# Optimization experiments

Measured on AMD Instinct MI355X. Metric: run time of the kernel, lower is better.

Reference implementation:

```python
import jax, jax.numpy as jnp
import numpy as np

KL_W, SIZ_W, DEN_W, MAT_W = 0.001, 0.05, 0.1, 0.1


def setup_inputs() -> dict:
    key = jax.random.key(0)
    ks = jax.random.split(key, 9)
    B, N, M, L = 4, 8192, 8192, 512
    return {
        "pred_pos": jax.random.normal(ks[0], (B, N, 3), jnp.float32),
        "pred_sizing": jax.random.normal(ks[1], (B, N, 1), jnp.float32),
        "pred_material": jax.random.normal(ks[2], (B, N, 4), jnp.float32),
        "target_pos": jax.random.normal(ks[3], (B, M, 3), jnp.float32),
        "target_sizing": jax.random.normal(ks[4], (B, N, 1), jnp.float32),
        "target_material": jax.random.normal(ks[5], (B, N, 4), jnp.float32),
        "mu": jax.random.normal(ks[6], (B, L), jnp.float32),
        "logvar": jax.random.normal(ks[7], (B, L), jnp.float32),
        "sub_idx": jax.random.randint(ks[8], (1024,), 0, N, jnp.int64),
    }


def _pairwise_sq(a, b):
    # squared euclidean distances: [B,N,M]
    a2 = jnp.sum(a * a, axis=-1)                     # [B,N]
    b2 = jnp.sum(b * b, axis=-1)                     # [B,M]
    ab = jnp.einsum('bnd,bmd->bnm', a, b)            # [B,N,M]
    return a2[:, :, None] + b2[:, None, :] - 2.0 * ab


def reference(pred_pos, pred_sizing, pred_material, target_pos,
              target_sizing, target_material, mu, logvar, sub_idx):
    # Chamfer: one pairwise matrix, min over both axes
    d = _pairwise_sq(pred_pos, target_pos)           # [B,N,M]
    cd = (jnp.min(d, axis=2).mean(axis=1) + jnp.min(d, axis=1).mean(axis=1)).mean()

    # KL divergence term
    kl = -0.5 * jnp.mean(1.0 + logvar - mu ** 2 - jnp.exp(logvar))

    # density uniformity on a 1024-point subsample
    pts = pred_pos[:, sub_idx]                       # [B,n,3]
    n = pts.shape[1]
    dd = _pairwise_sq(pts, pts) + jnp.eye(n, dtype=pts.dtype)[None] * 1e6
    nn_d = jnp.min(dd, axis=2)                       # [B,n]
    density = jnp.std(nn_d, axis=1, ddof=1).mean()   # torch .std is unbiased

    sizing_loss = jnp.mean((pred_sizing - target_sizing) ** 2)
    material_loss = jnp.mean((pred_material - target_material) ** 2)

    total = cd + KL_W * kl + DEN_W * density + SIZ_W * sizing_loss + MAT_W * material_loss
    return total
```

## Files before the change

### kernel.cpp

```cpp
#include <hip/hip_runtime.h>
#include <math.h>

#define BB 4
#define NN 8192
#define LL 512
#define NSUB 1024

#define AUX_BLOCKS 64
#define SL_BLOCKS 48
#define CH_BLOCKS 1024
#define PREP_BLOCKS 256

#define PPS_OFF 0
#define CHS_OFF 256
#define DNS_OFF 1280
#define KL_OFF  1312
#define SIZ_OFF 1360
#define MAT_OFF 1408
#define FRAG_OFF ((size_t)8192)
#define FRAG_SET ((size_t)BB * NN * 32)

typedef __bf16 bf16x8 __attribute__((ext_vector_type(8)));
typedef float f32x16 __attribute__((ext_vector_type(16)));

__device__ inline unsigned short f2bf(float f) {
    unsigned u = __float_as_uint(f);
    unsigned r = (u + 0x7FFFu + ((u >> 16) & 1u)) >> 16;
    return (unsigned short)r;
}
__device__ inline float bf2f(unsigned short h) {
    return __uint_as_float(((unsigned)h) << 16);
}
__device__ inline unsigned pk(unsigned short lo, unsigned short hi) {
    return (unsigned)lo | ((unsigned)hi << 16);
}

__device__ inline float blockReduceSum256(float v) {
    __shared__ float red[4];
    #pragma unroll
    for (int o = 32; o; o >>= 1) v += __shfl_down(v, o);
    __syncthreads();
    if ((threadIdx.x & 63) == 0) red[threadIdx.x >> 6] = v;
    __syncthreads();
    return red[0] + red[1] + red[2] + red[3];
}

__global__ __launch_bounds__(256) void prep_frags_kernel(
    const float* __restrict__ pred, const float* __restrict__ targ,
    unsigned char* __restrict__ frag, float* __restrict__ ws) {
    const int i = blockIdx.x * 256 + threadIdx.x;
    const int s = i >> 15;
    const int r = i & (BB * NN - 1);
    const int b = r >> 13;
    const int p = r & (NN - 1);
    const float* pos = (s ? targ : pred) + (size_t)r * 3;
    const float x = pos[0], y = pos[1], z = pos[2];
    const unsigned short hx = f2bf(x), hy = f2bf(y), hz = f2bf(z);
    const unsigned short lx = f2bf(x - bf2f(hx));
    const unsigned short ly = f2bf(y - bf2f(hy));
    const unsigned short lz = f2bf(z - bf2f(hz));
    const float pp = fmaf(x, x, fmaf(y, y, z * z));
    const float w = -0.5f * pp;
    const unsigned short wh = f2bf(w);
    const float wr = w - bf2f(wh);
    const unsigned short wl = f2bf(wr);
    const unsigned short wl2 = f2bf(wr - bf2f(wl));
    const unsigned short ONE = 0x3F80;

    uint4 a0, a1, b0, b1;
    a0.x = pk(hx, hy); a0.y = pk(hz, lx); a0.z = pk(ly, lz); a0.w = pk(hx, hy);
    a1.x = pk(hz, lx); a1.y = pk(ly, lz); a1.z = pk(ONE, ONE); a1.w = pk(ONE, 0);
    b0.x = pk(hx, hy); b0.y = pk(hz, hx); b0.z = pk(hy, hz); b0.w = pk(lx, ly);
    b1.x = pk(lz, lx); b1.y = pk(ly, lz); b1.z = pk(wh, wl); b1.w = pk(wl2, 0);

    uint4* Adst = (uint4*)(frag + (size_t)s * FRAG_SET) + (size_t)r * 2;
    Adst[0] = a0;
    Adst[1] = a1;
    uint4* Bdst = (uint4*)(frag + (2 + s) * FRAG_SET);
    const size_t bi = (size_t)b * NN * 2 + (size_t)(p >> 5) * 64 + (p & 31);
    Bdst[bi] = b0;
    Bdst[bi + 32] = b1;

    float sum = blockReduceSum256(pp);
    if (threadIdx.x == 0) ws[PPS_OFF + blockIdx.x] = sum;
}

__global__ __launch_bounds__(256, 4) void mega_kernel(
    const float* __restrict__ pred,
    const unsigned char* __restrict__ frag,
    const float* __restrict__ mu, const float* __restrict__ logvar,
    const float* __restrict__ psiz, const float* __restrict__ tsiz,
    const float* __restrict__ pmat, const float* __restrict__ tmat,
    const int* __restrict__ sub_idx, float* __restrict__ ws) {
    __shared__ __align__(16) unsigned char smem[16384];
    const int tid = threadIdx.x;
    const int bid = blockIdx.x;

    if (bid >= AUX_BLOCKS) {
        const int cid = bid - AUX_BLOCKS;
        const int bd = cid & 7;
        const int rg = cid >> 3;
        const int b = bd >> 1;
        const int dir = bd & 1;
        const int As = dir;
        const int Bs = dir ^ 1;
        const int w = tid >> 6, lane = tid & 63;
        const int lo5 = lane & 31, sel = lane >> 5;

        const uint4* Ap = (const uint4*)(frag + (size_t)As * FRAG_SET) +
                          (size_t)b * NN * 2;
        const int qbase = rg * 64;
        const bf16x8 A0 = __builtin_bit_cast(
            bf16x8, Ap[(size_t)(qbase + lo5) * 2 + sel]);
        const bf16x8 A1 = __builtin_bit_cast(
            bf16x8, Ap[(size_t)(qbase + 32 + lo5) * 2 + sel]);

        const uint4* Bq = (const uint4*)(frag + (size_t)(2 + Bs) * FRAG_SET) +
                          (size_t)b * NN * 2 + (size_t)w * 4096 + lane;

        f32x16 st0, st1;
        #pragma unroll
        for (int i = 0; i < 16; ++i) { st0[i] = -3e38f; st1[i] = -3e38f; }
        const f32x16 zc = {};

        uint4 c0 = Bq[0], c1 = Bq[64];
        uint4 n0 = Bq[128], n1 = Bq[192];
        #pragma unroll 1
        for (int it = 0; it < 32; ++it) {
            const int pf = (it < 30) ? (it + 2) : it;
            uint4 m0 = Bq[(size_t)pf * 128];
            uint4 m1 = Bq[(size_t)pf * 128 + 64];
            const bf16x8 B0 = __builtin_bit_cast(bf16x8, c0);
            const bf16x8 B1 = __builtin_bit_cast(bf16x8, c1);
            {
                f32x16 d0 = __builtin_amdgcn_mfma_f32_32x32x16_bf16(
                    A0, B0, zc, 0, 0, 0);
                f32x16 d1 = __builtin_amdgcn_mfma_f32_32x32x16_bf16(
                    A0, B1, zc, 0, 0, 0);
                #pragma unroll
                for (int i = 0; i < 16; ++i)
                    st0[i] = fmaxf(fmaxf(st0[i], d0[i]), d1[i]);
            }
            {
                f32x16 e0 = __builtin_amdgcn_mfma_f32_32x32x16_bf16(
                    A1, B0, zc, 0, 0, 0);
                f32x16 e1 = __builtin_amdgcn_mfma_f32_32x32x16_bf16(
                    A1, B1, zc, 0, 0, 0);
                #pragma unroll
                for (int i = 0; i < 16; ++i)
                    st1[i] = fmaxf(fmaxf(st1[i], e0[i]), e1[i]);
            }
            c0 = n0; c1 = n1;
            n0 = m0; n1 = m1;
        }

        #pragma unroll
        for (int m = 1; m <= 16; m <<= 1) {
            #pragma unroll
            for (int i = 0; i < 16; ++i) {
                st0[i] = fmaxf(st0[i], __shfl_xor(st0[i], m));
                st1[i] = fmaxf(st1[i], __shfl_xor(st1[i], m));
            }
        }
        float* sm = (float*)smem;
        if (lo5 == 0) {
            #pragma unroll
            for (int i = 0; i < 16; ++i) {
                const int r = (i & 3) + 8 * (i >> 2) + 4 * sel;
                sm[w * 64 + r] = st0[i];
                sm[w * 64 + 32 + r] = st1[i];
            }
        }
        __syncthreads();
        if (tid < 64) {
            float v = fmaxf(fmaxf(sm[tid], sm[64 + tid]),
                            fmaxf(sm[128 + tid], sm[192 + tid]));
            #pragma unroll
            for (int o = 32; o; o >>= 1) v += __shfl_down(v, o);
            if (tid == 0) ws[CHS_OFF + cid] = v;
        }
        return;
    }

    if (bid < 16) {
        float4* pts = (float4*)smem;
        const int chunk = bid & 3;
        const int b = bid >> 2;
        for (int k = tid; k < NSUB; k += 256) {
            int idx = sub_idx[k];
            const float* p = pred + ((size_t)b * NN + idx) * 3;
            float x = p[0], y = p[1], z = p[2];
            pts[k] = make_float4(x, y, z, -0.5f * fmaf(x, x, fmaf(y, y, z * z)));
        }
        __syncthreads();
        const int i = chunk * 256 + tid;
        const float4 me = pts[i];
        float h0 = -1e30f, h1 = -1e30f, h2 = -1e30f, h3 = -1e30f;
        #pragma unroll 4
        for (int j = 0; j < NSUB; j += 4) {
            float4 q0 = pts[j + 0], q1 = pts[j + 1], q2 = pts[j + 2], q3 = pts[j + 3];
            float t0 = fmaf(me.z, q0.z, q0.w);
            t0 = fmaf(me.y, q0.y, t0); t0 = fmaf(me.x, q0.x, t0);
            t0 = (j + 0 == i) ? -1e30f : t0; h0 = fmaxf(h0, t0);
            float t1 = fmaf(me.z, q1.z, q1.w);
            t1 = fmaf(me.y, q1.y, t1); t1 = fmaf(me.x, q1.x, t1);
            t1 = (j + 1 == i) ? -1e30f : t1; h1 = fmaxf(h1, t1);
            float t2 = fmaf(me.z, q2.z, q2.w);
            t2 = fmaf(me.y, q2.y, t2); t2 = fmaf(me.x, q2.x, t2);
            t2 = (j + 2 == i) ? -1e30f : t2; h2 = fmaxf(h2, t2);
            float t3 = fmaf(me.z, q3.z, q3.w);
            t3 = fmaf(me.y, q3.y, t3); t3 = fmaf(me.x, q3.x, t3);
            t3 = (j + 3 == i) ? -1e30f : t3; h3 = fmaxf(h3, t3);
        }
        float h = fmaxf(fmaxf(h0, h1), fmaxf(h2, h3));
        float pp = fmaf(me.x, me.x, fmaf(me.y, me.y, me.z * me.z));
        float m = pp - 2.0f * h;
        float s = blockReduceSum256(m); __syncthreads();
        float ss = blockReduceSum256(m * m);
        if (tid == 0) {
            ws[DNS_OFF + bid] = s;
            ws[DNS_OFF + 16 + bid] = ss;
        }
    } else {
        const int r = bid - 16;
        const int stride = SL_BLOCKS * 256;
        const int g0 = r * 256 + tid;
        float skl = 0.0f;
        for (int i = g0; i < BB * LL; i += stride) {
            float m = mu[i], lv = logvar[i];
            skl += 1.0f + lv - m * m - expf(lv);
        }
        float ssz = 0.0f;
        for (int i = g0; i < BB * NN; i += stride) {
            float d = psiz[i] - tsiz[i];
            ssz = fmaf(d, d, ssz);
        }
        float smt = 0.0f;
        for (int i = g0; i < BB * NN * 4; i += stride) {
            float d = pmat[i] - tmat[i];
            smt = fmaf(d, d, smt);
        }
        skl = blockReduceSum256(skl); __syncthreads();
        ssz = blockReduceSum256(ssz); __syncthreads();
        smt = blockReduceSum256(smt);
        if (tid == 0) {
            ws[KL_OFF + r] = skl;
            ws[SIZ_OFF + r] = ssz;
            ws[MAT_OFF + r] = smt;
        }
    }
}

__global__ __launch_bounds__(256) void finalize_kernel(
    const float* __restrict__ ws, float* __restrict__ out) {
    const int t = threadIdx.x;
    float pp = ws[PPS_OFF + t];
    float ch = ws[CHS_OFF + t] + ws[CHS_OFF + 256 + t] +
               ws[CHS_OFF + 512 + t] + ws[CHS_OFF + 768 + t];
    float kl = (t < SL_BLOCKS) ? ws[KL_OFF + t] : 0.0f;
    float sz = (t < SL_BLOCKS) ? ws[SIZ_OFF + t] : 0.0f;
    float mt = (t < SL_BLOCKS) ? ws[MAT_OFF + t] : 0.0f;
    float s_pp = blockReduceSum256(pp); __syncthreads();
    float s_ch = blockReduceSum256(ch); __syncthreads();
    float s_kl = blockReduceSum256(kl); __syncthreads();
    float s_sz = blockReduceSum256(sz); __syncthreads();
    float s_mt = blockReduceSum256(mt);
    if (t == 0) {
        float den = 0.0f;
        #pragma unroll
        for (int b = 0; b < BB; ++b) {
            float s = ws[DNS_OFF + 4 * b + 0] + ws[DNS_OFF + 4 * b + 1] +
                      ws[DNS_OFF + 4 * b + 2] + ws[DNS_OFF + 4 * b + 3];
            float q = ws[DNS_OFF + 16 + 4 * b + 0] + ws[DNS_OFF + 16 + 4 * b + 1] +
                      ws[DNS_OFF + 16 + 4 * b + 2] + ws[DNS_OFF + 16 + 4 * b + 3];
            float var = (q - s * s / (float)NSUB) / (float)(NSUB - 1);
            den += sqrtf(fmaxf(var, 0.0f));
        }
        den *= (1.0f / BB);
        float cd = (s_pp - 2.0f * s_ch) / (float)(BB * NN);
        float klv = -0.5f * s_kl / (float)(BB * LL);
        float sizing = s_sz / (float)(BB * NN);
        float material = s_mt / (float)(BB * NN * 4);
        out[0] = cd + 0.001f * klv + 0.1f * den + 0.05f * sizing +
                 0.1f * material;
    }
}

extern "C" void kernel_launch(void* const* d_in, const int* in_sizes, int n_in,
                              void* d_out, int out_size, void* d_ws,
                              size_t ws_size, hipStream_t stream) {
    const float* pred_pos = (const float*)d_in[0];
    const float* pred_siz = (const float*)d_in[1];
    const float* pred_mat = (const float*)d_in[2];
    const float* targ_pos = (const float*)d_in[3];
    const float* targ_siz = (const float*)d_in[4];
    const float* targ_mat = (const float*)d_in[5];
    const float* mu = (const float*)d_in[6];
    const float* logvar = (const float*)d_in[7];
    const int* sub_idx = (const int*)d_in[8];
    float* out = (float*)d_out;
    float* ws = (float*)d_ws;
    unsigned char* frag = (unsigned char*)d_ws + FRAG_OFF;

    prep_frags_kernel<<<PREP_BLOCKS, 256, 0, stream>>>(pred_pos, targ_pos,
                                                       frag, ws);
    mega_kernel<<<AUX_BLOCKS + CH_BLOCKS, 256, 0, stream>>>(
        pred_pos, frag, mu, logvar, pred_siz, targ_siz, pred_mat, targ_mat,
        sub_idx, ws);
    finalize_kernel<<<1, 256, 0, stream>>>(ws, out);
}
```

Measured before the change: 42.28 us.

## Move aux work into prep kernel and give chamfer its own kernel

The density and small-loss (KL, sizing, material) blocks move out of the chamfer mega-kernel into the prep kernel. Chamfer then runs as a dedicated kernel with a lean 1 KB shared buffer instead of 16 KB. Its block index mapping also changes so consecutive blocks share the same batch and direction, which should improve L2 reuse of the B fragments. This removes the imbalance of aux blocks competing with MFMA blocks, at the cost of a longer prep kernel.

```diff
diff --git a/kernel.cpp b/kernel.cpp
--- a/kernel.cpp
+++ b/kernel.cpp
@@ -6,10 +6,10 @@
 #define LL 512
 #define NSUB 1024
 
-#define AUX_BLOCKS 64
 #define SL_BLOCKS 48
 #define CH_BLOCKS 1024
-#define PREP_BLOCKS 256
+#define PREP_BLOCKS 320
+#define RED_BLOCKS 64
 
 #define PPS_OFF 0
 #define CHS_OFF 256
@@ -45,147 +45,57 @@
     return red[0] + red[1] + red[2] + red[3];
 }
 
-__global__ __launch_bounds__(256) void prep_frags_kernel(
+__global__ __launch_bounds__(256) void prep_kernel(
     const float* __restrict__ pred, const float* __restrict__ targ,
-    unsigned char* __restrict__ frag, float* __restrict__ ws) {
-    const int i = blockIdx.x * 256 + threadIdx.x;
-    const int s = i >> 15;
-    const int r = i & (BB * NN - 1);
-    const int b = r >> 13;
-    const int p = r & (NN - 1);
-    const float* pos = (s ? targ : pred) + (size_t)r * 3;
-    const float x = pos[0], y = pos[1], z = pos[2];
-    const unsigned short hx = f2bf(x), hy = f2bf(y), hz = f2bf(z);
-    const unsigned short lx = f2bf(x - bf2f(hx));
-    const unsigned short ly = f2bf(y - bf2f(hy));
-    const unsigned short lz = f2bf(z - bf2f(hz));
-    const float pp = fmaf(x, x, fmaf(y, y, z * z));
-    const float w = -0.5f * pp;
-    const unsigned short wh = f2bf(w);
-    const float wr = w - bf2f(wh);
-    const unsigned short wl = f2bf(wr);
-    const unsigned short wl2 = f2bf(wr - bf2f(wl));
-    const unsigned short ONE = 0x3F80;
-
-    uint4 a0, a1, b0, b1;
-    a0.x = pk(hx, hy); a0.y = pk(hz, lx); a0.z = pk(ly, lz); a0.w = pk(hx, hy);
-    a1.x = pk(hz, lx); a1.y = pk(ly, lz); a1.z = pk(ONE, ONE); a1.w = pk(ONE, 0);
-    b0.x = pk(hx, hy); b0.y = pk(hz, hx); b0.z = pk(hy, hz); b0.w = pk(lx, ly);
-    b1.x = pk(lz, lx); b1.y = pk(ly, lz); b1.z = pk(wh, wl); b1.w = pk(wl2, 0);
-
-    uint4* Adst = (uint4*)(frag + (size_t)s * FRAG_SET) + (size_t)r * 2;
-    Adst[0] = a0;
-    Adst[1] = a1;
-    uint4* Bdst = (uint4*)(frag + (2 + s) * FRAG_SET);
-    const size_t bi = (size_t)b * NN * 2 + (size_t)(p >> 5) * 64 + (p & 31);
-    Bdst[bi] = b0;
-    Bdst[bi + 32] = b1;
-
-    float sum = blockReduceSum256(pp);
-    if (threadIdx.x == 0) ws[PPS_OFF + blockIdx.x] = sum;
-}
-
-__global__ __launch_bounds__(256, 4) void mega_kernel(
-    const float* __restrict__ pred,
-    const unsigned char* __restrict__ frag,
+    unsigned char* __restrict__ frag,
     const float* __restrict__ mu, const float* __restrict__ logvar,
     const float* __restrict__ psiz, const float* __restrict__ tsiz,
     const float* __restrict__ pmat, const float* __restrict__ tmat,
     const int* __restrict__ sub_idx, float* __restrict__ ws) {
-    __shared__ __align__(16) unsigned char smem[16384];
+    __shared__ __align__(16) float4 pts[NSUB];
     const int tid = threadIdx.x;
     const int bid = blockIdx.x;
 
-    if (bid >= AUX_BLOCKS) {
-        const int cid = bid - AUX_BLOCKS;
-        const int bd = cid & 7;
-        const int rg = cid >> 3;
-        const int b = bd >> 1;
-        const int dir = bd & 1;
-        const int As = dir;
-        const int Bs = dir ^ 1;
-        const int w = tid >> 6, lane = tid & 63;
-        const int lo5 = lane & 31, sel = lane >> 5;
-
-        const uint4* Ap = (const uint4*)(frag + (size_t)As * FRAG_SET) +
-                          (size_t)b * NN * 2;
-        const int qbase = rg * 64;
-        const bf16x8 A0 = __builtin_bit_cast(
-            bf16x8, Ap[(size_t)(qbase + lo5) * 2 + sel]);
-        const bf16x8 A1 = __builtin_bit_cast(
-            bf16x8, Ap[(size_t)(qbase + 32 + lo5) * 2 + sel]);
-
-        const uint4* Bq = (const uint4*)(frag + (size_t)(2 + Bs) * FRAG_SET) +
-                          (size_t)b * NN * 2 + (size_t)w * 4096 + lane;
-
-        f32x16 st0, st1;
-        #pragma unroll
-        for (int i = 0; i < 16; ++i) { st0[i] = -3e38f; st1[i] = -3e38f; }
-        const f32x16 zc = {};
-
-        uint4 c0 = Bq[0], c1 = Bq[64];
-        uint4 n0 = Bq[128], n1 = Bq[192];
-        #pragma unroll 1
-        for (int it = 0; it < 32; ++it) {
-            const int pf = (it < 30) ? (it + 2) : it;
-            uint4 m0 = Bq[(size_t)pf * 128];
-            uint4 m1 = Bq[(size_t)pf * 128 + 64];
-            const bf16x8 B0 = __builtin_bit_cast(bf16x8, c0);
-            const bf16x8 B1 = __builtin_bit_cast(bf16x8, c1);
-            {
-                f32x16 d0 = __builtin_amdgcn_mfma_f32_32x32x16_bf16(
-                    A0, B0, zc, 0, 0, 0);
-                f32x16 d1 = __builtin_amdgcn_mfma_f32_32x32x16_bf16(
-                    A0, B1, zc, 0, 0, 0);
-                #pragma unroll
-                for (int i = 0; i < 16; ++i)
-                    st0[i] = fmaxf(fmaxf(st0[i], d0[i]), d1[i]);
-            }
-            {
-                f32x16 e0 = __builtin_amdgcn_mfma_f32_32x32x16_bf16(
-                    A1, B0, zc, 0, 0, 0);
-                f32x16 e1 = __builtin_amdgcn_mfma_f32_32x32x16_bf16(
-                    A1, B1, zc, 0, 0, 0);
-                #pragma unroll
-                for (int i = 0; i < 16; ++i)
-                    st1[i] = fmaxf(fmaxf(st1[i], e0[i]), e1[i]);
-            }
-            c0 = n0; c1 = n1;
-            n0 = m0; n1 = m1;
-        }
-
-        #pragma unroll
-        for (int m = 1; m <= 16; m <<= 1) {
-            #pragma unroll
-            for (int i = 0; i < 16; ++i) {
-                st0[i] = fmaxf(st0[i], __shfl_xor(st0[i], m));
-                st1[i] = fmaxf(st1[i], __shfl_xor(st1[i], m));
-            }
-        }
-        float* sm = (float*)smem;
-        if (lo5 == 0) {
-            #pragma unroll
-            for (int i = 0; i < 16; ++i) {
-                const int r = (i & 3) + 8 * (i >> 2) + 4 * sel;
-                sm[w * 64 + r] = st0[i];
-                sm[w * 64 + 32 + r] = st1[i];
-            }
-        }
-        __syncthreads();
-        if (tid < 64) {
-            float v = fmaxf(fmaxf(sm[tid], sm[64 + tid]),
-                            fmaxf(sm[128 + tid], sm[192 + tid]));
-            #pragma unroll
-            for (int o = 32; o; o >>= 1) v += __shfl_down(v, o);
-            if (tid == 0) ws[CHS_OFF + cid] = v;
-        }
-        return;
-    }
-
-    if (bid < 16) {
-        float4* pts = (float4*)smem;
-        const int chunk = bid & 3;
-        const int b = bid >> 2;
+    if (bid < 256) {
+        const int i = bid * 256 + tid;
+        const int s = i >> 15;
+        const int r = i & (BB * NN - 1);
+        const int b = r >> 13;
+        const int p = r & (NN - 1);
+        const float* pos = (s ? targ : pred) + (size_t)r * 3;
+        const float x = pos[0], y = pos[1], z = pos[2];
+        const unsigned short hx = f2bf(x), hy = f2bf(y), hz = f2bf(z);
+        const unsigned short lx = f2bf(x - bf2f(hx));
+        const unsigned short ly = f2bf(y - bf2f(hy));
+        const unsigned short lz = f2bf(z - bf2f(hz));
+        const float pp = fmaf(x, x, fmaf(y, y, z * z));
+        const float w = -0.5f * pp;
+        const unsigned short wh = f2bf(w);
+        const float wr = w - bf2f(wh);
+        const unsigned short wl = f2bf(wr);
+        const unsigned short wl2 = f2bf(wr - bf2f(wl));
+        const unsigned short ONE = 0x3F80;
+
+        uint4 a0, a1, b0, b1;
+        a0.x = pk(hx, hy); a0.y = pk(hz, lx); a0.z = pk(ly, lz); a0.w = pk(hx, hy);
+        a1.x = pk(hz, lx); a1.y = pk(ly, lz); a1.z = pk(ONE, ONE); a1.w = pk(ONE, 0);
+        b0.x = pk(hx, hy); b0.y = pk(hz, hx); b0.z = pk(hy, hz); b0.w = pk(lx, ly);
+        b1.x = pk(lz, lx); b1.y = pk(ly, lz); b1.z = pk(wh, wl); b1.w = pk(wl2, 0);
+
+        uint4* Adst = (uint4*)(frag + (size_t)s * FRAG_SET) + (size_t)r * 2;
+        Adst[0] = a0;
+        Adst[1] = a1;
+        uint4* Bdst = (uint4*)(frag + (2 + s) * FRAG_SET);
+        const size_t bi = (size_t)b * NN * 2 + (size_t)(p >> 5) * 64 + (p & 31);
+        Bdst[bi] = b0;
+        Bdst[bi + 32] = b1;
+
+        float sum = blockReduceSum256(pp);
+        if (tid == 0) ws[PPS_OFF + bid] = sum;
+    } else if (bid < 272) {
+        const int v = bid - 256;
+        const int chunk = v & 3;
+        const int b = v >> 2;
         for (int k = tid; k < NSUB; k += 256) {
             int idx = sub_idx[k];
             const float* p = pred + ((size_t)b * NN + idx) * 3;
@@ -218,11 +128,11 @@
         float s = blockReduceSum256(m); __syncthreads();
         float ss = blockReduceSum256(m * m);
         if (tid == 0) {
-            ws[DNS_OFF + bid] = s;
-            ws[DNS_OFF + 16 + bid] = ss;
+            ws[DNS_OFF + v] = s;
+            ws[DNS_OFF + 16 + v] = ss;
         }
     } else {
-        const int r = bid - 16;
+        const int r = bid - 272;
         const int stride = SL_BLOCKS * 256;
         const int g0 = r * 256 + tid;
         float skl = 0.0f;
@@ -248,6 +158,93 @@
             ws[SIZ_OFF + r] = ssz;
             ws[MAT_OFF + r] = smt;
         }
+    }
+}
+
+__global__ __launch_bounds__(256, 4) void chamfer_kernel(
+    const unsigned char* __restrict__ frag, float* __restrict__ ws) {
+    __shared__ __align__(16) float sm[256];
+    const int tid = threadIdx.x;
+    const int cid = blockIdx.x;
+    const int rg = cid & 127;
+    const int bd = cid >> 7;
+    const int b = bd >> 1;
+    const int dir = bd & 1;
+    const int As = dir;
+    const int Bs = dir ^ 1;
+    const int w = tid >> 6, lane = tid & 63;
+    const int lo5 = lane & 31, sel = lane >> 5;
+
+    const uint4* Ap = (const uint4*)(frag + (size_t)As * FRAG_SET) +
+                      (size_t)b * NN * 2;
+    const int qbase = rg * 64;
+    const bf16x8 A0 = __builtin_bit_cast(
+        bf16x8, Ap[(size_t)(qbase + lo5) * 2 + sel]);
+    const bf16x8 A1 = __builtin_bit_cast(
+        bf16x8, Ap[(size_t)(qbase + 32 + lo5) * 2 + sel]);
+
+    const uint4* Bq = (const uint4*)(frag + (size_t)(2 + Bs) * FRAG_SET) +
+                      (size_t)b * NN * 2 + (size_t)w * 4096 + lane;
+
+    f32x16 st0, st1;
+    #pragma unroll
+    for (int i = 0; i < 16; ++i) { st0[i] = -3e38f; st1[i] = -3e38f; }
+    const f32x16 zc = {};
+
+    uint4 c0 = Bq[0], c1 = Bq[64];
+    uint4 n0 = Bq[128], n1 = Bq[192];
+    #pragma unroll 1
+    for (int it = 0; it < 32; ++it) {
+        const int pf = (it < 30) ? (it + 2) : it;
+        uint4 m0 = Bq[(size_t)pf * 128];
+        uint4 m1 = Bq[(size_t)pf * 128 + 64];
+        const bf16x8 B0 = __builtin_bit_cast(bf16x8, c0);
+        const bf16x8 B1 = __builtin_bit_cast(bf16x8, c1);
+        {
+            f32x16 d0 = __builtin_amdgcn_mfma_f32_32x32x16_bf16(
+                A0, B0, zc, 0, 0, 0);
+            f32x16 d1 = __builtin_amdgcn_mfma_f32_32x32x16_bf16(
+                A0, B1, zc, 0, 0, 0);
+            #pragma unroll
+            for (int i = 0; i < 16; ++i)
+                st0[i] = fmaxf(fmaxf(st0[i], d0[i]), d1[i]);
+        }
+        {
+            f32x16 e0 = __builtin_amdgcn_mfma_f32_32x32x16_bf16(
+                A1, B0, zc, 0, 0, 0);
+            f32x16 e1 = __builtin_amdgcn_mfma_f32_32x32x16_bf16(
+                A1, B1, zc, 0, 0, 0);
+            #pragma unroll
+            for (int i = 0; i < 16; ++i)
+                st1[i] = fmaxf(fmaxf(st1[i], e0[i]), e1[i]);
+        }
+        c0 = n0; c1 = n1;
+        n0 = m0; n1 = m1;
+    }
+
+    #pragma unroll
+    for (int m = 1; m <= 16; m <<= 1) {
+        #pragma unroll
+        for (int i = 0; i < 16; ++i) {
+            st0[i] = fmaxf(st0[i], __shfl_xor(st0[i], m));
+            st1[i] = fmaxf(st1[i], __shfl_xor(st1[i], m));
+        }
+    }
+    if (lo5 == 0) {
+        #pragma unroll
+        for (int i = 0; i < 16; ++i) {
+            const int r = (i & 3) + 8 * (i >> 2) + 4 * sel;
+            sm[w * 64 + r] = st0[i];
+            sm[w * 64 + 32 + r] = st1[i];
+        }
+    }
+    __syncthreads();
+    if (tid < 64) {
+        float v = fmaxf(fmaxf(sm[tid], sm[64 + tid]),
+                        fmaxf(sm[128 + tid], sm[192 + tid]));
+        #pragma unroll
+        for (int o = 32; o; o >>= 1) v += __shfl_down(v, o);
+        if (tid == 0) ws[CHS_OFF + cid] = v;
     }
 }
 
@@ -302,10 +299,9 @@
     float* ws = (float*)d_ws;
     unsigned char* frag = (unsigned char*)d_ws + FRAG_OFF;
 
-    prep_frags_kernel<<<PREP_BLOCKS, 256, 0, stream>>>(pred_pos, targ_pos,
-                                                       frag, ws);
-    mega_kernel<<<AUX_BLOCKS + CH_BLOCKS, 256, 0, stream>>>(
-        pred_pos, frag, mu, logvar, pred_siz, targ_siz, pred_mat, targ_mat,
-        sub_idx, ws);
+    prep_kernel<<<PREP_BLOCKS, 256, 0, stream>>>(
+        pred_pos, targ_pos, frag, mu, logvar, pred_siz, targ_siz, pred_mat,
+        targ_mat, sub_idx, ws);
+    chamfer_kernel<<<CH_BLOCKS, 256, 0, stream>>>(frag, ws);
     finalize_kernel<<<1, 256, 0, stream>>>(ws, out);
 }
```

Result: slower. 54.46 us (+28.8%).

## Double Chamfer query tile per block to 128 rows, halving block count

Applied to the files above, without the earlier changes.

Each Chamfer block now keeps four A fragments (128 query points) in registers instead of two, so every loaded B fragment feeds eight MFMAs rather than four. The chamfer block count is halved and the workspace offsets and finalize reduction are adjusted to match. Block-to-work mapping is changed so consecutive blocks share batch and direction. The aim is to cut global B-fragment traffic per MFMA; the costs are higher register pressure (launch bounds lowered to 3 blocks per SM) and fewer blocks for a GPU with many CUs.

```diff
diff --git a/kernel.cpp b/kernel.cpp
--- a/kernel.cpp
+++ b/kernel.cpp
@@ -8,15 +8,15 @@
 
 #define AUX_BLOCKS 64
 #define SL_BLOCKS 48
-#define CH_BLOCKS 1024
+#define CH_BLOCKS 512
 #define PREP_BLOCKS 256
 
 #define PPS_OFF 0
 #define CHS_OFF 256
-#define DNS_OFF 1280
-#define KL_OFF  1312
-#define SIZ_OFF 1360
-#define MAT_OFF 1408
+#define DNS_OFF 768
+#define KL_OFF  800
+#define SIZ_OFF 848
+#define MAT_OFF 896
 #define FRAG_OFF ((size_t)8192)
 #define FRAG_SET ((size_t)BB * NN * 32)
 
@@ -85,7 +85,7 @@
     if (threadIdx.x == 0) ws[PPS_OFF + blockIdx.x] = sum;
 }
 
-__global__ __launch_bounds__(256, 4) void mega_kernel(
+__global__ __launch_bounds__(256, 3) void mega_kernel(
     const float* __restrict__ pred,
     const unsigned char* __restrict__ frag,
     const float* __restrict__ mu, const float* __restrict__ logvar,
@@ -98,8 +98,8 @@
 
     if (bid >= AUX_BLOCKS) {
         const int cid = bid - AUX_BLOCKS;
-        const int bd = cid & 7;
-        const int rg = cid >> 3;
+        const int rg = cid & 63;
+        const int bd = cid >> 6;
         const int b = bd >> 1;
         const int dir = bd & 1;
         const int As = dir;
@@ -109,49 +109,110 @@
 
         const uint4* Ap = (const uint4*)(frag + (size_t)As * FRAG_SET) +
                           (size_t)b * NN * 2;
-        const int qbase = rg * 64;
+        const int qbase = rg * 128;
         const bf16x8 A0 = __builtin_bit_cast(
             bf16x8, Ap[(size_t)(qbase + lo5) * 2 + sel]);
         const bf16x8 A1 = __builtin_bit_cast(
             bf16x8, Ap[(size_t)(qbase + 32 + lo5) * 2 + sel]);
+        const bf16x8 A2 = __builtin_bit_cast(
+            bf16x8, Ap[(size_t)(qbase + 64 + lo5) * 2 + sel]);
+        const bf16x8 A3 = __builtin_bit_cast(
+            bf16x8, Ap[(size_t)(qbase + 96 + lo5) * 2 + sel]);
 
         const uint4* Bq = (const uint4*)(frag + (size_t)(2 + Bs) * FRAG_SET) +
                           (size_t)b * NN * 2 + (size_t)w * 4096 + lane;
 
-        f32x16 st0, st1;
+        f32x16 st0, st1, st2, st3;
         #pragma unroll
-        for (int i = 0; i < 16; ++i) { st0[i] = -3e38f; st1[i] = -3e38f; }
+        for (int i = 0; i < 16; ++i) {
+            st0[i] = -3e38f; st1[i] = -3e38f;
+            st2[i] = -3e38f; st3[i] = -3e38f;
+        }
         const f32x16 zc = {};
 
-        uint4 c0 = Bq[0], c1 = Bq[64];
-        uint4 n0 = Bq[128], n1 = Bq[192];
+        uint4 r0a = Bq[0],   r0b = Bq[64];
+        uint4 r1a = Bq[128], r1b = Bq[192];
+
         #pragma unroll 1
-        for (int it = 0; it < 32; ++it) {
-            const int pf = (it < 30) ? (it + 2) : it;
-            uint4 m0 = Bq[(size_t)pf * 128];
-            uint4 m1 = Bq[(size_t)pf * 128 + 64];
-            const bf16x8 B0 = __builtin_bit_cast(bf16x8, c0);
-            const bf16x8 B1 = __builtin_bit_cast(bf16x8, c1);
+        for (int c = 0; c < 16; ++c) {
             {
-                f32x16 d0 = __builtin_amdgcn_mfma_f32_32x32x16_bf16(
-                    A0, B0, zc, 0, 0, 0);
-                f32x16 d1 = __builtin_amdgcn_mfma_f32_32x32x16_bf16(
-                    A0, B1, zc, 0, 0, 0);
-                #pragma unroll
-                for (int i = 0; i < 16; ++i)
-                    st0[i] = fmaxf(fmaxf(st0[i], d0[i]), d1[i]);
+                const int nx = (2 * c + 2 < 32) ? (2 * c + 2) : (2 * c);
+                const bf16x8 B0 = __builtin_bit_cast(bf16x8, r0a);
+                const bf16x8 B1 = __builtin_bit_cast(bf16x8, r0b);
+                {
+                    f32x16 d = __builtin_amdgcn_mfma_f32_32x32x16_bf16(A0, B0, zc, 0, 0, 0);
+                    #pragma unroll
+                    for (int i = 0; i < 16; ++i) st0[i] = fmaxf(st0[i], d[i]);
+                    d = __builtin_amdgcn_mfma_f32_32x32x16_bf16(A0, B1, zc, 0, 0, 0);
+                    #pragma unroll
+                    for (int i = 0; i < 16; ++i) st0[i] = fmaxf(st0[i], d[i]);
+                }
+                {
+                    f32x16 d = __builtin_amdgcn_mfma_f32_32x32x16_bf16(A1, B0, zc, 0, 0, 0);
+                    #pragma unroll
+                    for (int i = 0; i < 16; ++i) st1[i] = fmaxf(st1[i], d[i]);
+                    d = __builtin_amdgcn_mfma_f32_32x32x16_bf16(A1, B1, zc, 0, 0, 0);
+                    #pragma unroll
+                    for (int i = 0; i < 16; ++i) st1[i] = fmaxf(st1[i], d[i]);
+                }
+                r0a = Bq[(size_t)nx * 128];
+                r0b = Bq[(size_t)nx * 128 + 64];
+                {
+                    f32x16 d = __builtin_amdgcn_mfma_f32_32x32x16_bf16(A2, B0, zc, 0, 0, 0);
+                    #pragma unroll
+                    for (int i = 0; i < 16; ++i) st2[i] = fmaxf(st2[i], d[i]);
+                    d = __builtin_amdgcn_mfma_f32_32x32x16_bf16(A2, B1, zc, 0, 0, 0);
+                    #pragma unroll
+                    for (int i = 0; i < 16; ++i) st2[i] = fmaxf(st2[i], d[i]);
+                }
+                {
+                    f32x16 d = __builtin_amdgcn_mfma_f32_32x32x16_bf16(A3, B0, zc, 0, 0, 0);
+                    #pragma unroll
+                    for (int i = 0; i < 16; ++i) st3[i] = fmaxf(st3[i], d[i]);
+                    d = __builtin_amdgcn_mfma_f32_32x32x16_bf16(A3, B1, zc, 0, 0, 0);
+                    #pragma unroll
+                    for (int i = 0; i < 16; ++i) st3[i] = fmaxf(st3[i], d[i]);
+                }
             }
             {
-                f32x16 e0 = __builtin_amdgcn_mfma_f32_32x32x16_bf16(
-                    A1, B0, zc, 0, 0, 0);
-                f32x16 e1 = __builtin_amdgcn_mfma_f32_32x32x16_bf16(
-                    A1, B1, zc, 0, 0, 0);
-                #pragma unroll
-                for (int i = 0; i < 16; ++i)
-                    st1[i] = fmaxf(fmaxf(st1[i], e0[i]), e1[i]);
+                const int nx = (2 * c + 3 < 32) ? (2 * c + 3) : (2 * c + 1);
+                const bf16x8 B0 = __builtin_bit_cast(bf16x8, r1a);
+                const bf16x8 B1 = __builtin_bit_cast(bf16x8, r1b);
+                {
+                    f32x16 d = __builtin_amdgcn_mfma_f32_32x32x16_bf16(A0, B0, zc, 0, 0, 0);
+                    #pragma unroll
+                    for (int i = 0; i < 16; ++i) st0[i] = fmaxf(st0[i], d[i]);
+                    d = __builtin_amdgcn_mfma_f32_32x32x16_bf16(A0, B1, zc, 0, 0, 0);
+                    #pragma unroll
+                    for (int i = 0; i < 16; ++i) st0[i] = fmaxf(st0[i], d[i]);
+                }
+                {
+                    f32x16 d = __builtin_amdgcn_mfma_f32_32x32x16_bf16(A1, B0, zc, 0, 0, 0);
+                    #pragma unroll
+                    for (int i = 0; i < 16; ++i) st1[i] = fmaxf(st1[i], d[i]);
+                    d = __builtin_amdgcn_mfma_f32_32x32x16_bf16(A1, B1, zc, 0, 0, 0);
+                    #pragma unroll
+                    for (int i = 0; i < 16; ++i) st1[i] = fmaxf(st1[i], d[i]);
+                }
+                r1a = Bq[(size_t)nx * 128];
+                r1b = Bq[(size_t)nx * 128 + 64];
+                {
+                    f32x16 d = __builtin_amdgcn_mfma_f32_32x32x16_bf16(A2, B0, zc, 0, 0, 0);
+                    #pragma unroll
+                    for (int i = 0; i < 16; ++i) st2[i] = fmaxf(st2[i], d[i]);
+                    d = __builtin_amdgcn_mfma_f32_32x32x16_bf16(A2, B1, zc, 0, 0, 0);
+                    #pragma unroll
+                    for (int i = 0; i < 16; ++i) st2[i] = fmaxf(st2[i], d[i]);
+                }
+                {
+                    f32x16 d = __builtin_amdgcn_mfma_f32_32x32x16_bf16(A3, B0, zc, 0, 0, 0);
+                    #pragma unroll
+                    for (int i = 0; i < 16; ++i) st3[i] = fmaxf(st3[i], d[i]);
+                    d = __builtin_amdgcn_mfma_f32_32x32x16_bf16(A3, B1, zc, 0, 0, 0);
+                    #pragma unroll
+                    for (int i = 0; i < 16; ++i) st3[i] = fmaxf(st3[i], d[i]);
+                }
             }
-            c0 = n0; c1 = n1;
-            n0 = m0; n1 = m1;
         }
 
         #pragma unroll
@@ -160,6 +221,8 @@
             for (int i = 0; i < 16; ++i) {
                 st0[i] = fmaxf(st0[i], __shfl_xor(st0[i], m));
                 st1[i] = fmaxf(st1[i], __shfl_xor(st1[i], m));
+                st2[i] = fmaxf(st2[i], __shfl_xor(st2[i], m));
+                st3[i] = fmaxf(st3[i], __shfl_xor(st3[i], m));
             }
         }
         float* sm = (float*)smem;
@@ -167,18 +230,21 @@
             #pragma unroll
             for (int i = 0; i < 16; ++i) {
                 const int r = (i & 3) + 8 * (i >> 2) + 4 * sel;
-                sm[w * 64 + r] = st0[i];
-                sm[w * 64 + 32 + r] = st1[i];
+                sm[w * 128 + r] = st0[i];
+                sm[w * 128 + 32 + r] = st1[i];
+                sm[w * 128 + 64 + r] = st2[i];
+                sm[w * 128 + 96 + r] = st3[i];
             }
         }
         __syncthreads();
-        if (tid < 64) {
-            float v = fmaxf(fmaxf(sm[tid], sm[64 + tid]),
-                            fmaxf(sm[128 + tid], sm[192 + tid]));
-            #pragma unroll
-            for (int o = 32; o; o >>= 1) v += __shfl_down(v, o);
-            if (tid == 0) ws[CHS_OFF + cid] = v;
-        }
+        float v = 0.0f;
+        if (tid < 128) {
+            v = fmaxf(fmaxf(sm[tid], sm[128 + tid]),
+                      fmaxf(sm[256 + tid], sm[384 + tid]));
+        }
+        __syncthreads();
+        float s = blockReduceSum256(v);
+        if (tid == 0) ws[CHS_OFF + cid] = s;
         return;
     }
 
@@ -255,8 +321,7 @@
     const float* __restrict__ ws, float* __restrict__ out) {
     const int t = threadIdx.x;
     float pp = ws[PPS_OFF + t];
-    float ch = ws[CHS_OFF + t] + ws[CHS_OFF + 256 + t] +
-               ws[CHS_OFF + 512 + t] + ws[CHS_OFF + 768 + t];
+    float ch = ws[CHS_OFF + t] + ws[CHS_OFF + 256 + t];
     float kl = (t < SL_BLOCKS) ? ws[KL_OFF + t] : 0.0f;
     float sz = (t < SL_BLOCKS) ? ws[SIZ_OFF + t] : 0.0f;
     float mt = (t < SL_BLOCKS) ? ws[MAT_OFF + t] : 0.0f;
```

Result: slower. 75.52 us (+78.6%).
